# Kernel tuning notes

Hardware: AMD Instinct MI355X
Metric: run time of the kernel (lower is better)

The kernel has to match this reference:

```python
import jax, jax.numpy as jnp
import numpy as np
import math

B, T, D = 2, 2048, 2048
N_HEADS, N_KV_HEADS = 16, 4
HEAD_DIM = D // N_HEADS          # 128
N_GROUPS = N_HEADS // N_KV_HEADS # 4


def setup_inputs() -> dict:
    key = jax.random.key(0)
    k1, k2, k3, k4, k5 = jax.random.split(key, 5)
    x = jax.random.normal(k1, (B, T, D), dtype=jnp.float32)
    # RoPE table: [T, head_dim//2, 2] = (cos, sin)
    inv_freq = 1.0 / (10000.0 ** (np.arange(0, HEAD_DIM, 2, dtype=np.float32) / HEAD_DIM))
    ang = np.arange(T, dtype=np.float32)[:, None] * inv_freq[None, :]  # [T, hd/2]
    rope = jnp.asarray(np.stack([np.cos(ang), np.sin(ang)], axis=-1), dtype=jnp.float32)
    s = 0.02
    wq = s * jax.random.normal(k2, (N_HEADS * HEAD_DIM, D), dtype=jnp.float32)
    wk = s * jax.random.normal(k3, (N_KV_HEADS * HEAD_DIM, D), dtype=jnp.float32)
    wv = s * jax.random.normal(k4, (N_KV_HEADS * HEAD_DIM, D), dtype=jnp.float32)
    wo = s * jax.random.normal(k5, (D, D), dtype=jnp.float32)
    return {"x": x, "rope": rope, "wq": wq, "wk": wk, "wv": wv, "wo": wo}


def apply_rope(t, rope):
    # t: [B, H, T, hd]; rope: [T, hd/2, 2]
    d = t.shape[-1]
    t1, t2 = t[..., : d // 2], t[..., d // 2 :]
    cos = rope[..., 0][None, None]  # [1,1,T,hd/2]
    sin = rope[..., 1][None, None]
    return jnp.concatenate([t1 * cos - t2 * sin, t1 * sin + t2 * cos], axis=-1)


def reference(x, rope, wq, wk, wv, wo):
    b, t, c = x.shape
    q = (x @ wq.T).reshape(b, t, N_HEADS, HEAD_DIM).transpose(0, 2, 1, 3)
    k = (x @ wk.T).reshape(b, t, N_KV_HEADS, HEAD_DIM).transpose(0, 2, 1, 3)
    v = (x @ wv.T).reshape(b, t, N_KV_HEADS, HEAD_DIM).transpose(0, 2, 1, 3)
    q = apply_rope(q, rope)
    k = apply_rope(k, rope)
    k = jnp.repeat(k, N_GROUPS, axis=1)  # [B, H, T, hd]
    v = jnp.repeat(v, N_GROUPS, axis=1)
    scale = 1.0 / math.sqrt(HEAD_DIM)
    scores = jnp.einsum("bhqd,bhkd->bhqk", q, k) * scale
    causal = jnp.tril(jnp.ones((t, t), dtype=bool))
    scores = jnp.where(causal[None, None], scores, jnp.finfo(scores.dtype).min)
    attn = jax.nn.softmax(scores, axis=-1)
    y = jnp.einsum("bhqk,bhkd->bhqd", attn, v)
    y = y.transpose(0, 2, 1, 3).reshape(b, t, c)
    return y @ wo.T
```

## Files before the change

### kernel.cpp

```cpp
#include <hip/hip_runtime.h>

typedef unsigned short u16;
typedef float   f32x4  __attribute__((ext_vector_type(4)));
typedef short   short8 __attribute__((ext_vector_type(8)));
typedef __bf16  bf16x8 __attribute__((ext_vector_type(8)));
typedef float   float4v __attribute__((ext_vector_type(4)));
typedef unsigned short u16x4 __attribute__((ext_vector_type(4)));

static __device__ __forceinline__ u16 f2b(float f) {
  union { float f; unsigned u; } v; v.f = f;
  unsigned r = (v.u + 0x7fffu + ((v.u >> 16) & 1u)) >> 16;
  return (u16)r;
}
static __device__ __forceinline__ float b2f(u16 h) {
  union { unsigned u; float f; } v; v.u = ((unsigned)h) << 16;
  return v.f;
}
static __device__ __forceinline__ f32x4 mfma_bf16(short8 a, short8 b, f32x4 c) {
  return __builtin_amdgcn_mfma_f32_16x16x32_bf16(
      __builtin_bit_cast(bf16x8, a), __builtin_bit_cast(bf16x8, b), c, 0, 0, 0);
}
static __device__ __forceinline__ void gload_lds16(const u16* g, u16* l) {
  __builtin_amdgcn_global_load_lds(
      (const __attribute__((address_space(1))) unsigned int*)g,
      (__attribute__((address_space(3))) unsigned int*)l, 16, 0, 0);
}

#define BB 2
#define TT 2048
#define DD 2048
#define NH 16
#define NKVH 4
#define HD 128
#define MM (BB * TT)
#define QSTR 3072

#define N4_X   ((MM * DD) / 4)
#define N4_WQ  ((DD * DD) / 4)
#define N4_WKV ((NKVH * HD * DD) / 4)
#define N4_WO  ((DD * DD) / 4)
#define N4_TOT (N4_X + N4_WQ + 2 * N4_WKV + N4_WO)

__global__ __launch_bounds__(256) void cvt_all(const float* __restrict__ x,
                                               const float* __restrict__ wq,
                                               const float* __restrict__ wk,
                                               const float* __restrict__ wv,
                                               const float* __restrict__ wo,
                                               u16* __restrict__ xb,
                                               u16* __restrict__ wqkvb,
                                               u16* __restrict__ wob) {
  int stride = gridDim.x * blockDim.x;
  for (int i = blockIdx.x * blockDim.x + threadIdx.x; i < N4_TOT; i += stride) {
    const float4v* src;
    u16x4* dst;
    int off;
    if (i < N4_X) {
      src = (const float4v*)x; dst = (u16x4*)xb; off = i;
    } else if (i < N4_X + N4_WQ) {
      src = (const float4v*)wq; dst = (u16x4*)wqkvb; off = i - N4_X;
    } else if (i < N4_X + N4_WQ + N4_WKV) {
      src = (const float4v*)wk; dst = (u16x4*)wqkvb + N4_WQ; off = i - (N4_X + N4_WQ);
    } else if (i < N4_X + N4_WQ + 2 * N4_WKV) {
      src = (const float4v*)wv; dst = (u16x4*)wqkvb + N4_WQ + N4_WKV;
      off = i - (N4_X + N4_WQ + N4_WKV);
    } else {
      src = (const float4v*)wo; dst = (u16x4*)wob; off = i - (N4_X + N4_WQ + 2 * N4_WKV);
    }
    float4v v = src[off];
    u16x4 o;
    o[0] = f2b(v[0]); o[1] = f2b(v[1]); o[2] = f2b(v[2]); o[3] = f2b(v[3]);
    dst[off] = o;
  }
}

#define ROPE_QN (MM * NH * 64)

static __device__ __forceinline__ void rope_one(u16* X, const float* rope,
                                                int idx, int n_heads, float scale) {
  int i  = idx & 63;
  int h  = (idx >> 6) % n_heads;
  int bt = idx / (64 * n_heads);
  int t  = bt & (TT - 1);
  size_t base = (size_t)bt * QSTR + h * HD + i;
  float x1 = b2f(X[base]);
  float x2 = b2f(X[base + 64]);
  float c = rope[t * 128 + 2 * i];
  float s = rope[t * 128 + 2 * i + 1];
  X[base]      = f2b(scale * (x1 * c - x2 * s));
  X[base + 64] = f2b(scale * (x1 * s + x2 * c));
}

__global__ __launch_bounds__(256) void rope_all(u16* __restrict__ QKV,
                                                const float* __restrict__ rope) {
  int idx = blockIdx.x * 256 + threadIdx.x;
  if (idx < ROPE_QN)
    rope_one(QKV, rope, idx, NH, 0.08838834764831845f);
  else
    rope_one(QKV + DD, rope, idx - ROPE_QN, NKVH, 1.0f);
}

template <bool OUTBF>
__global__ __launch_bounds__(256) void gemm_bt(const u16* __restrict__ A,
                                               const u16* __restrict__ W,
                                               void* __restrict__ Cout,
                                               int M, int N, int K) {
  __shared__ __align__(16) u16 As[128 * 32];
  __shared__ __align__(16) u16 Ws[128 * 32];
  const int tid = threadIdx.x, lane = tid & 63, wid = tid >> 6;
  const int wr = wid >> 1, wc = wid & 1;
  const int brow = blockIdx.y * 128, bcol = blockIdx.x * 128;
  const int l15 = lane & 15, lh = lane >> 4;

  const int c0 = wid * 64 + lane;
  const int c1 = c0 + 256;
  const u16* Ag0 = A + (size_t)(brow + (c0 >> 2)) * K + ((c0 & 3) << 3);
  const u16* Ag1 = A + (size_t)(brow + (c1 >> 2)) * K + ((c1 & 3) << 3);
  const u16* Wg0 = W + (size_t)(bcol + (c0 >> 2)) * K + ((c0 & 3) << 3);
  const u16* Wg1 = W + (size_t)(bcol + (c1 >> 2)) * K + ((c1 & 3) << 3);
  u16* lA0 = &As[(wid * 64) * 8];
  u16* lA1 = &As[(wid * 64 + 256) * 8];
  u16* lW0 = &Ws[(wid * 64) * 8];
  u16* lW1 = &Ws[(wid * 64 + 256) * 8];

  f32x4 acc[4][4];
#pragma unroll
  for (int m = 0; m < 4; ++m)
#pragma unroll
    for (int n = 0; n < 4; ++n) acc[m][n] = (f32x4)0.0f;

  for (int k0 = 0; k0 < K; k0 += 32) {
    __syncthreads();
    gload_lds16(Ag0 + k0, lA0);
    gload_lds16(Ag1 + k0, lA1);
    gload_lds16(Wg0 + k0, lW0);
    gload_lds16(Wg1 + k0, lW1);
    __syncthreads();
    short8 af[4], bfr[4];
#pragma unroll
    for (int m = 0; m < 4; ++m)
      af[m] = *(const short8*)&As[(wr * 64 + m * 16 + l15) * 32 + (lh << 3)];
#pragma unroll
    for (int n = 0; n < 4; ++n)
      bfr[n] = *(const short8*)&Ws[(wc * 64 + n * 16 + l15) * 32 + (lh << 3)];
#pragma unroll
    for (int m = 0; m < 4; ++m)
#pragma unroll
      for (int n = 0; n < 4; ++n)
        acc[m][n] = mfma_bf16(af[m], bfr[n], acc[m][n]);
  }

#pragma unroll
  for (int m = 0; m < 4; ++m)
#pragma unroll
    for (int n = 0; n < 4; ++n)
#pragma unroll
      for (int j = 0; j < 4; ++j) {
        int row = brow + wr * 64 + m * 16 + lh * 4 + j;
        int col = bcol + wc * 64 + n * 16 + l15;
        if (OUTBF)
          ((u16*)Cout)[(size_t)row * N + col] = f2b(acc[m][n][j]);
        else
          ((float*)Cout)[(size_t)row * N + col] = acc[m][n][j];
      }
}

#define QBLK 128
#define KVBLK 128

static __device__ __forceinline__ void attn_tile(
    const short8* qa, f32x4* o, f32x4& ol, float* mrow,
    int qrow0, int kv0,
    const u16* Ks, const unsigned* Vt32, u16* myP,
    int l15, int lh, short8 ones8) {
  if (kv0 > qrow0 + 15) return;

  f32x4 s[4];
#pragma unroll
  for (int nt = 0; nt < 4; ++nt) s[nt] = (f32x4)0.0f;
  __builtin_amdgcn_s_setprio(1);
#pragma unroll
  for (int nt = 0; nt < 4; ++nt)
#pragma unroll
    for (int kk = 0; kk < 4; ++kk) {
      short8 kb = *(const short8*)&Ks[(nt * 16 + l15) * 136 + kk * 32 + (lh << 3)];
      s[nt] = mfma_bf16(qa[kk], kb, s[nt]);
    }
  __builtin_amdgcn_s_setprio(0);

  const int qg = qrow0 + lh * 4;
#pragma unroll
  for (int j = 0; j < 4; ++j)
#pragma unroll
    for (int nt = 0; nt < 4; ++nt)
      if (kv0 + nt * 16 + l15 > qg + j) s[nt][j] = -1e30f;

  float mt[4];
#pragma unroll
  for (int j = 0; j < 4; ++j)
    mt[j] = fmaxf(fmaxf(s[0][j], s[1][j]), fmaxf(s[2][j], s[3][j]));
#pragma unroll
  for (int d = 1; d <= 8; d <<= 1)
#pragma unroll
    for (int j = 0; j < 4; ++j) mt[j] = fmaxf(mt[j], __shfl_xor(mt[j], d));

  float gmax = mt[0] - mrow[0];
#pragma unroll
  for (int j = 1; j < 4; ++j) gmax = fmaxf(gmax, mt[j] - mrow[j]);
  if (!__all(gmax <= 8.0f)) {
#pragma unroll
    for (int j = 0; j < 4; ++j) {
      float mn = fmaxf(mrow[j], mt[j]);
      float a = __expf(mrow[j] - mn);
      mrow[j] = mn;
      ol[j] *= a;
#pragma unroll
      for (int n = 0; n < 8; ++n) o[n][j] *= a;
    }
  }

  f32x4 p[4];
#pragma unroll
  for (int nt = 0; nt < 4; ++nt)
#pragma unroll
    for (int j = 0; j < 4; ++j) p[nt][j] = __expf(s[nt][j] - mrow[j]);

#pragma unroll
  for (int nt = 0; nt < 4; ++nt)
#pragma unroll
    for (int j = 0; j < 4; ++j)
      myP[(lh * 4 + j) * 72 + nt * 16 + l15] = f2b(p[nt][j]);

  __builtin_amdgcn_s_setprio(1);
#pragma unroll
  for (int c = 0; c < 2; ++c) {
    short8 pa = *(const short8*)&myP[l15 * 72 + c * 32 + (lh << 3)];
    ol = mfma_bf16(pa, ones8, ol);
#pragma unroll
    for (int nt2 = 0; nt2 < 8; ++nt2) {
      int d = nt2 * 16 + l15;
      int byteoff = (d * 144 + (c * 32 + lh * 8) * 2) ^ (((d >> 3) & 7) << 4);
      short8 vb = *(const short8*)((const char*)Vt32 + byteoff);
      o[nt2] = mfma_bf16(pa, vb, o[nt2]);
    }
  }
  __builtin_amdgcn_s_setprio(0);
}

__global__ __launch_bounds__(512) void attn_kernel(const u16* __restrict__ QKV,
                                                   u16* __restrict__ Y) {
  __shared__ __align__(16) u16 Ks[2][64 * 136];
  __shared__ __align__(16) unsigned Vt32[2][128 * 36];
  __shared__ __align__(16) u16 Ps[8][16 * 72];

  const int tid = threadIdx.x, lane = tid & 63, wid = tid >> 6;
  const int l15 = lane & 15, lh = lane >> 4;
  const int bid = blockIdx.x;
  const int qpair = bid & 7;
  const int h = (bid >> 3) & 15;
  const int b = bid >> 7;
  const int kvh = h >> 2;
  const int qtA = qpair, qtB = 15 - qpair;
  const int rowA = qtA * QBLK + wid * 16;
  const int rowB = qtB * QBLK + wid * 16;

  const u16* Kb_ = QKV + (size_t)b * TT * QSTR + DD + kvh * HD;
  const u16* Vb_ = Kb_ + NKVH * HD;

  short8 ones8;
#pragma unroll
  for (int e = 0; e < 8; ++e) ones8[e] = (short)0x3F80;

  short8 qaA[4], qaB[4];
  {
    const u16* qA = QKV + (size_t)(b * TT + rowA + l15) * QSTR + h * HD + (lh << 3);
    const u16* qB = QKV + (size_t)(b * TT + rowB + l15) * QSTR + h * HD + (lh << 3);
#pragma unroll
    for (int kk = 0; kk < 4; ++kk) {
      qaA[kk] = *(const short8*)(qA + kk * 32);
      qaB[kk] = *(const short8*)(qB + kk * 32);
    }
  }

  f32x4 oA[8], oB[8];
  f32x4 olA = (f32x4)0.0f, olB = (f32x4)0.0f;
  float mA[4], mB[4];
#pragma unroll
  for (int n = 0; n < 8; ++n) { oA[n] = (f32x4)0.0f; oB[n] = (f32x4)0.0f; }
#pragma unroll
  for (int j = 0; j < 4; ++j) { mA[j] = -1e30f; mB[j] = -1e30f; }

  const int kvend = (qtB + 1) * QBLK;

  short8 kreg[4], vreg[4];
  const int srow = tid >> 4;
  const int sc8 = (tid & 15) << 3;

  auto issue = [&](int kv0) {
    kreg[0] = *(const short8*)&Kb_[(size_t)(kv0 + srow) * QSTR + sc8];
    kreg[1] = *(const short8*)&Kb_[(size_t)(kv0 + 32 + srow) * QSTR + sc8];
    kreg[2] = *(const short8*)&Kb_[(size_t)(kv0 + 64 + srow) * QSTR + sc8];
    kreg[3] = *(const short8*)&Kb_[(size_t)(kv0 + 96 + srow) * QSTR + sc8];
    vreg[0] = *(const short8*)&Vb_[(size_t)(kv0 + 2 * srow) * QSTR + sc8];
    vreg[1] = *(const short8*)&Vb_[(size_t)(kv0 + 2 * srow + 1) * QSTR + sc8];
    vreg[2] = *(const short8*)&Vb_[(size_t)(kv0 + 64 + 2 * srow) * QSTR + sc8];
    vreg[3] = *(const short8*)&Vb_[(size_t)(kv0 + 64 + 2 * srow + 1) * QSTR + sc8];
  };

  issue(0);
  for (int kv0 = 0; kv0 < kvend; kv0 += KVBLK) {
    __syncthreads();
    *(short8*)&Ks[0][srow * 136 + sc8] = kreg[0];
    *(short8*)&Ks[0][(srow + 32) * 136 + sc8] = kreg[1];
    *(short8*)&Ks[1][srow * 136 + sc8] = kreg[2];
    *(short8*)&Ks[1][(srow + 32) * 136 + sc8] = kreg[3];
#pragma unroll
    for (int e = 0; e < 8; ++e) {
      int d = sc8 + e;
      unsigned pk0 = (unsigned)(u16)vreg[0][e] | ((unsigned)(u16)vreg[1][e] << 16);
      unsigned pk1 = (unsigned)(u16)vreg[2][e] | ((unsigned)(u16)vreg[3][e] << 16);
      int byteoff = (d * 144 + 4 * srow) ^ (((d >> 3) & 7) << 4);
      *(unsigned*)((char*)&Vt32[0][0] + byteoff) = pk0;
      *(unsigned*)((char*)&Vt32[1][0] + byteoff) = pk1;
    }
    __syncthreads();
    if (kv0 + KVBLK < kvend) issue(kv0 + KVBLK);

    attn_tile(qaA, oA, olA, mA, rowA, kv0,      &Ks[0][0], &Vt32[0][0], &Ps[wid][0], l15, lh, ones8);
    attn_tile(qaA, oA, olA, mA, rowA, kv0 + 64, &Ks[1][0], &Vt32[1][0], &Ps[wid][0], l15, lh, ones8);
    attn_tile(qaB, oB, olB, mB, rowB, kv0,      &Ks[0][0], &Vt32[0][0], &Ps[wid][0], l15, lh, ones8);
    attn_tile(qaB, oB, olB, mB, rowB, kv0 + 64, &Ks[1][0], &Vt32[1][0], &Ps[wid][0], l15, lh, ones8);
  }

  f32x4 invA, invB;
#pragma unroll
  for (int j = 0; j < 4; ++j) {
    invA[j] = __builtin_amdgcn_rcpf(olA[j]);
    invB[j] = __builtin_amdgcn_rcpf(olB[j]);
  }
#pragma unroll
  for (int nt = 0; nt < 8; ++nt)
#pragma unroll
    for (int j = 0; j < 4; ++j) {
      Y[(size_t)(b * TT + rowA + lh * 4 + j) * DD + h * HD + nt * 16 + l15] =
          f2b(oA[nt][j] * invA[j]);
      Y[(size_t)(b * TT + rowB + lh * 4 + j) * DD + h * HD + nt * 16 + l15] =
          f2b(oB[nt][j] * invB[j]);
    }
}

extern "C" void kernel_launch(void* const* d_in, const int* in_sizes, int n_in,
                              void* d_out, int out_size, void* d_ws, size_t ws_size,
                              hipStream_t stream) {
  const float* x    = (const float*)d_in[0];
  const float* rope = (const float*)d_in[1];
  const float* wq   = (const float*)d_in[2];
  const float* wk   = (const float*)d_in[3];
  const float* wv   = (const float*)d_in[4];
  const float* wo   = (const float*)d_in[5];
  float* out = (float*)d_out;

  char* ws = (char*)d_ws;
  u16* xb    = (u16*)ws; ws += (size_t)MM * DD * 2;
  u16* wqkvb = (u16*)ws; ws += (size_t)QSTR * DD * 2;
  u16* wob   = (u16*)ws; ws += (size_t)DD * DD * 2;
  u16* QKVb  = (u16*)ws; ws += (size_t)MM * QSTR * 2;
  u16* Yb    = (u16*)ws;

  cvt_all<<<2048, 256, 0, stream>>>(x, wq, wk, wv, wo, xb, wqkvb, wob);

  gemm_bt<true><<<dim3(QSTR / 128, MM / 128), 256, 0, stream>>>(xb, wqkvb, QKVb, MM, QSTR, DD);

  rope_all<<<(ROPE_QN + MM * NKVH * 64) / 256, 256, 0, stream>>>(QKVb, rope);

  attn_kernel<<<BB * NH * (TT / QBLK / 2), 512, 0, stream>>>(QKVb, Yb);

  gemm_bt<false><<<dim3(DD / 128, MM / 128), 256, 0, stream>>>(Yb, wob, out, MM, DD, DD);
}
```

Measured before the change: 232.9 us.

## Fuse Q RoPE into attention, swizzle GEMM block order, use native bf16 convert

```diff
diff --git a/kernel.cpp b/kernel.cpp
--- a/kernel.cpp
+++ b/kernel.cpp
@@ -8,9 +8,7 @@
 typedef unsigned short u16x4 __attribute__((ext_vector_type(4)));
 
 static __device__ __forceinline__ u16 f2b(float f) {
-  union { float f; unsigned u; } v; v.f = f;
-  unsigned r = (v.u + 0x7fffu + ((v.u >> 16) & 1u)) >> 16;
-  return (u16)r;
+  return __builtin_bit_cast(u16, (__bf16)f);
 }
 static __device__ __forceinline__ float b2f(u16 h) {
   union { unsigned u; float f; } v; v.u = ((unsigned)h) << 16;
@@ -34,6 +32,7 @@
 #define HD 128
 #define MM (BB * TT)
 #define QSTR 3072
+#define QSCALE 0.08838834764831845f
 
 #define N4_X   ((MM * DD) / 4)
 #define N4_WQ  ((DD * DD) / 4)
@@ -73,30 +72,20 @@
   }
 }
 
-#define ROPE_QN (MM * NH * 64)
-
-static __device__ __forceinline__ void rope_one(u16* X, const float* rope,
-                                                int idx, int n_heads, float scale) {
+__global__ __launch_bounds__(256) void rope_k(u16* __restrict__ K,
+                                              const float* __restrict__ rope) {
+  int idx = blockIdx.x * 256 + threadIdx.x;
   int i  = idx & 63;
-  int h  = (idx >> 6) % n_heads;
-  int bt = idx / (64 * n_heads);
+  int h  = (idx >> 6) & (NKVH - 1);
+  int bt = idx >> 8;
   int t  = bt & (TT - 1);
   size_t base = (size_t)bt * QSTR + h * HD + i;
-  float x1 = b2f(X[base]);
-  float x2 = b2f(X[base + 64]);
+  float x1 = b2f(K[base]);
+  float x2 = b2f(K[base + 64]);
   float c = rope[t * 128 + 2 * i];
   float s = rope[t * 128 + 2 * i + 1];
-  X[base]      = f2b(scale * (x1 * c - x2 * s));
-  X[base + 64] = f2b(scale * (x1 * s + x2 * c));
-}
-
-__global__ __launch_bounds__(256) void rope_all(u16* __restrict__ QKV,
-                                                const float* __restrict__ rope) {
-  int idx = blockIdx.x * 256 + threadIdx.x;
-  if (idx < ROPE_QN)
-    rope_one(QKV, rope, idx, NH, 0.08838834764831845f);
-  else
-    rope_one(QKV + DD, rope, idx - ROPE_QN, NKVH, 1.0f);
+  K[base]      = f2b(x1 * c - x2 * s);
+  K[base + 64] = f2b(x1 * s + x2 * c);
 }
 
 template <bool OUTBF>
@@ -108,7 +97,11 @@
   __shared__ __align__(16) u16 Ws[128 * 32];
   const int tid = threadIdx.x, lane = tid & 63, wid = tid >> 6;
   const int wr = wid >> 1, wc = wid & 1;
-  const int brow = blockIdx.y * 128, bcol = blockIdx.x * 128;
+  const int gx = gridDim.x;
+  const int lin = blockIdx.y * gx + blockIdx.x;
+  const int cpx = (gx * gridDim.y) >> 3;
+  const int swz = (lin & 7) * cpx + (lin >> 3);
+  const int brow = (swz / gx) * 128, bcol = (swz % gx) * 128;
   const int l15 = lane & 15, lh = lane >> 4;
 
   const int c0 = wid * 64 + lane;
@@ -247,6 +240,7 @@
 }
 
 __global__ __launch_bounds__(512) void attn_kernel(const u16* __restrict__ QKV,
+                                                   const float* __restrict__ rope,
                                                    u16* __restrict__ Y) {
   __shared__ __align__(16) u16 Ks[2][64 * 136];
   __shared__ __align__(16) unsigned Vt32[2][128 * 36];
@@ -280,6 +274,24 @@
       qaB[kk] = *(const short8*)(qB + kk * 32);
     }
   }
+  {
+    const float* rpA = rope + (size_t)(rowA + l15) * 128;
+    const float* rpB = rope + (size_t)(rowB + l15) * 128;
+#pragma unroll
+    for (int kk = 0; kk < 2; ++kk)
+#pragma unroll
+      for (int e = 0; e < 8; ++e) {
+        const int i2 = 2 * (kk * 32 + (lh << 3) + e);
+        float c = rpA[i2], s = rpA[i2 + 1];
+        float x1 = b2f((u16)qaA[kk][e]), x2 = b2f((u16)qaA[kk + 2][e]);
+        qaA[kk][e]     = (short)f2b(QSCALE * (x1 * c - x2 * s));
+        qaA[kk + 2][e] = (short)f2b(QSCALE * (x1 * s + x2 * c));
+        float cb = rpB[i2], sb = rpB[i2 + 1];
+        float y1 = b2f((u16)qaB[kk][e]), y2 = b2f((u16)qaB[kk + 2][e]);
+        qaB[kk][e]     = (short)f2b(QSCALE * (y1 * cb - y2 * sb));
+        qaB[kk + 2][e] = (short)f2b(QSCALE * (y1 * sb + y2 * cb));
+      }
+  }
 
   f32x4 oA[8], oB[8];
   f32x4 olA = (f32x4)0.0f, olB = (f32x4)0.0f;
@@ -370,9 +382,9 @@
 
   gemm_bt<true><<<dim3(QSTR / 128, MM / 128), 256, 0, stream>>>(xb, wqkvb, QKVb, MM, QSTR, DD);
 
-  rope_all<<<(ROPE_QN + MM * NKVH * 64) / 256, 256, 0, stream>>>(QKVb, rope);
-
-  attn_kernel<<<BB * NH * (TT / QBLK / 2), 512, 0, stream>>>(QKVb, Yb);
+  rope_k<<<(MM * NKVH * 64) / 256, 256, 0, stream>>>(QKVb + DD, rope);
+
+  attn_kernel<<<BB * NH * (TT / QBLK / 2), 512, 0, stream>>>(QKVb, rope, Yb);
 
   gemm_bt<false><<<dim3(DD / 128, MM / 128), 256, 0, stream>>>(Yb, wob, out, MM, DD, DD);
 }
```

New measurement: 226.6 us. 1.03x faster.
